# Kernel tuning notes

Measured on AMD Instinct MI355X. Metric: run time of the kernel, lower is better.

The kernel has to match this reference:

```python
import jax, jax.numpy as jnp
import numpy as np

E = 8            # moe_num_experts
HIDDEN = 1024    # hidden_size
FFN = 4096       # ffn_hidden_size
TOKENS = 8192    # total tokens, pre-sorted by expert; balanced -> TOKENS // E per expert


def setup_inputs() -> dict:
    key = jax.random.key(0)
    k1, k2, k3 = jax.random.split(key, 3)
    x = jax.random.normal(k1, (TOKENS, HIDDEN), dtype=jnp.float32)
    # w1, w2 stored flattened as [E*FFN, HIDDEN], matching create_dmoe_expert_weights' view([-1, columns])
    w1 = jax.random.normal(k2, (E * FFN, HIDDEN), dtype=jnp.float32) * (1.0 / np.sqrt(HIDDEN))
    w2 = jax.random.normal(k3, (E * FFN, HIDDEN), dtype=jnp.float32) * (1.0 / np.sqrt(FFN))
    return {"x": x, "w1": w1, "w2": w2, "num_experts": E}


def reference(x, w1, w2, num_experts):
    # Block-diagonal topology of dMoE SparseMLP: tokens sorted by expert, each
    # expert owns a contiguous FFN slice of w1/w2. Equivalent grouped GEMM:
    #   out_e = gelu(x_e @ w1_e^T) @ w2_e   (megablocks gelu = tanh-approx GELU)
    tokens, hidden = x.shape
    ffn = w1.shape[0] // num_experts
    tpe = tokens // num_experts  # tokens per expert (balanced topology)
    xe = x.reshape(num_experts, tpe, hidden)        # [E, T/E, H]
    w1e = w1.reshape(num_experts, ffn, hidden)      # [E, F, H]
    w2e = w2.reshape(num_experts, ffn, hidden)      # [E, F, H]
    h = jax.nn.gelu(jnp.einsum('eth,efh->etf', xe, w1e), approximate=True)  # sdd + gelu
    out = jnp.einsum('etf,efh->eth', h, w2e)        # dsd
    return out.reshape(tokens, hidden)
```

## Files before the change

kernel.cpp:

```cpp
#include <hip/hip_runtime.h>
#include <hip/hip_bf16.h>
#include <stdint.h>

#define NE 8
#define HID 1024
#define FFN 4096
#define TOK 8192
#define TPE (TOK / NE)

typedef __attribute__((ext_vector_type(8))) short    bf16x8;
typedef __attribute__((ext_vector_type(4))) float    f32x4;
typedef __attribute__((ext_vector_type(4))) unsigned short ushort4v;
typedef __attribute__((ext_vector_type(8))) unsigned short ushort8v;


__device__ __forceinline__ unsigned short f2bf(float f) {
    union { float f; unsigned u; } c; c.f = f;
    unsigned r = c.u + 0x7fffu + ((c.u >> 16) & 1u);
    return (unsigned short)(r >> 16);
}

__device__ __forceinline__ float gelu_tanh(float x) {
    const float c0 = 0.7978845608028654f;
    const float c1 = 0.044715f;
    float u = c0 * (x + c1 * x * x * x);
    float t = 1.0f - 2.0f / (1.0f + __expf(2.0f * u));
    return 0.5f * x * (1.0f + t);
}

typedef const __attribute__((address_space(1))) void gbl_void_t;
typedef __attribute__((address_space(3))) void lds_void_t;

__device__ __forceinline__ void gload_lds16(const void* g, void* l) {
    __builtin_amdgcn_global_load_lds((gbl_void_t*)g, (lds_void_t*)l, 16, 0, 0);
}


__global__ void cvt_f32_bf16(const float* __restrict__ in,
                             unsigned short* __restrict__ out) {
    size_t i = ((size_t)blockIdx.x * blockDim.x + threadIdx.x) * 8;
    f32x4 a = *(const f32x4*)(in + i);
    f32x4 b = *(const f32x4*)(in + i + 4);
    ushort8v o;
#pragma unroll
    for (int j = 0; j < 4; j++) { o[j] = f2bf(a[j]); o[4 + j] = f2bf(b[j]); }
    *(ushort8v*)(out + i) = o;
}


__global__ void transpose_cvt(const float* __restrict__ in,
                              unsigned short* __restrict__ out) {
    __shared__ unsigned short tile[64][65];
    const int e  = blockIdx.z;
    const int f0 = blockIdx.x * 64;
    const int h0 = blockIdx.y * 64;
    const float*     src = in  + (size_t)e * FFN * HID;
    unsigned short*  dst = out + (size_t)e * HID * FFN;
    const int t  = threadIdx.x;
    const int tr = t >> 4;
    const int tc = (t & 15) * 4;
#pragma unroll
    for (int i = 0; i < 4; i++) {
        int f = i * 16 + tr;
        f32x4 v = *(const f32x4*)(src + (size_t)(f0 + f) * HID + h0 + tc);
#pragma unroll
        for (int j = 0; j < 4; j++) tile[f][tc + j] = f2bf(v[j]);
    }
    __syncthreads();
#pragma unroll
    for (int i = 0; i < 4; i++) {
        int h = i * 16 + tr;
        ushort4v o;
#pragma unroll
        for (int j = 0; j < 4; j++) o[j] = tile[tc + j][h];
        *(ushort4v*)(dst + (size_t)(h0 + h) * FFN + f0 + tc) = o;
    }
}


template <int BN, int GX, int GY, bool GELU>
__global__ __launch_bounds__(512, 2)
void gemm8p(const unsigned short* __restrict__ A,
            const unsigned short* __restrict__ B,
            void* __restrict__ Cout, int M, int N, int K) {
    constexpr int BM = 256, BK = 64;
    constexpr int NH = BN / 128;
    constexpr int NI = 2 * NH;
    constexpr int LB = BN / 128;
    constexpr int S  = BN / 8;
    constexpr int ABYTES = BM * BK * 2;
    constexpr int BBYTES = BN * BK * 2;
    constexpr int BUF = ABYTES + BBYTES;
    constexpr int VMC = 2 + 2 * LB;
    constexpr int NWG = NE * GX * GY;

    __shared__ __align__(16) char lds[2 * BUF];

    const int lin = blockIdx.x;
    const int wid = (lin & 7) * (NWG >> 3) + (lin >> 3);
    const int e   = wid / (GX * GY);
    const int rem = wid % (GX * GY);
    const int m0  = (rem % GX) * BM;
    const int n0  = (rem / GX) * BN;

    const size_t K2 = (size_t)K * 2;
    const char* Ae = (const char*)(A + (size_t)e * M * K);
    const char* Be = (const char*)(B + (size_t)e * N * K);

    const int tid  = threadIdx.x;
    const int lane = tid & 63;
    const int w    = tid >> 6;
    const int wr   = w >> 2, wc = w & 3;
    const int fr   = lane & 15, fq = lane >> 4;

    const int rA  = tid >> 3;
    const int kb  = (tid & 7) * 16;
    const int kbs = kb ^ ((rA & 7) << 4);
    const char* aptr = Ae + (size_t)(m0 + rA) * K2 + kbs;
    const int   fB   = (rA / S) * 2 * S + (rA % S);
    const char* bptr = Be + (size_t)(n0 + fB) * K2 + kbs;
    char* dA0 = lds + rA * 128 + kb;
    char* dA1 = dA0 + BUF;
    char* dB0 = lds + ABYTES + fB * 128 + kb;
    char* dB1 = dB0 + BUF;

    auto SA = [&](int au, int kt, char* d) {
        const char* s = aptr + (size_t)kt * 128;
#pragma unroll
        for (int i = 0; i < 2; i++)
            gload_lds16(s + (size_t)(au * 64 + i * 128) * K2,
                        d + (au * 64 + i * 128) * 128);
    };
    auto SB = [&](int bu, int kt, char* d) {
        const char* s = bptr + (size_t)kt * 128;
#pragma unroll
        for (int i = 0; i < LB; i++)
            gload_lds16(s + (size_t)(bu * S + i * 128) * K2,
                        d + (bu * S + i * 128) * 128);
    };

    const int kx0 = (fq * 16) ^ ((lane & 7) << 4);
    const char* paA = lds + (wr * 128 + fr) * 128;
    const char* paB = lds + ABYTES + (wc * (BN / 4) + fr) * 128;
    const char* pa0k0 = paA + kx0;        const char* pa0k1 = paA + (kx0 ^ 64);
    const char* pa1k0 = pa0k0 + BUF;      const char* pa1k1 = pa0k1 + BUF;
    const char* pb0k0 = paB + kx0;        const char* pb0k1 = paB + (kx0 ^ 64);
    const char* pb1k0 = pb0k0 + BUF;      const char* pb1k1 = pb0k1 + BUF;

    f32x4 acc[8][NI];
#pragma unroll
    for (int i = 0; i < 8; i++)
#pragma unroll
        for (int j = 0; j < NI; j++) acc[i][j] = f32x4{0.f, 0.f, 0.f, 0.f};

    bf16x8 a[4][2], b0[NH][2], b1[NH][2];

    auto LDA = [&](const char* p0, const char* p1, int mq) {
#pragma unroll
        for (int mi = 0; mi < 4; mi++) {
            a[mi][0] = *(const bf16x8*)(p0 + mq * 8192 + mi * 2048);
            a[mi][1] = *(const bf16x8*)(p1 + mq * 8192 + mi * 2048);
        }
    };
    auto LDB = [&](const char* p0, const char* p1, int nq, bf16x8 (&bb)[NH][2]) {
#pragma unroll
        for (int ni = 0; ni < NH; ni++) {
            bb[ni][0] = *(const bf16x8*)(p0 + (nq * (BN / 8) + ni * 16) * 128);
            bb[ni][1] = *(const bf16x8*)(p1 + (nq * (BN / 8) + ni * 16) * 128);
        }
    };
    auto MMQ = [&](int mq, int nq, bf16x8 (&bb)[NH][2]) {
        __builtin_amdgcn_s_setprio(1);
#pragma unroll
        for (int mi = 0; mi < 4; mi++)
#pragma unroll
            for (int ni = 0; ni < NH; ni++) {
                f32x4& c = acc[mq * 4 + mi][nq * NH + ni];
                c = __builtin_amdgcn_mfma_f32_16x16x32_bf16(a[mi][0], bb[ni][0], c, 0, 0, 0);
                c = __builtin_amdgcn_mfma_f32_16x16x32_bf16(a[mi][1], bb[ni][1], c, 0, 0, 0);
            }
        __builtin_amdgcn_s_setprio(0);
    };

#define MIDBAR()  __builtin_amdgcn_s_barrier();                                      \
                  asm volatile("s_waitcnt lgkmcnt(0)" ::: "memory");                 \
                  __builtin_amdgcn_sched_barrier(0)
#define ENDBAR()  __builtin_amdgcn_s_barrier();                                      \
                  __builtin_amdgcn_sched_barrier(0)
#define LGHINT()  asm volatile("s_waitcnt lgkmcnt(8)" ::: "memory")
#define VMW()     asm volatile("s_waitcnt vmcnt(%0)" :: "n"(VMC) : "memory")

    const int NT   = K / BK;
    const int NTm1 = NT - 1;

    SA(0, 0, dA0); SB(0, 0, dB0); SB(1, 0, dB0); SA(1, 0, dA0);
    SA(0, 1, dA1); SB(0, 1, dB1); SB(1, 1, dB1);
    VMW();
    __builtin_amdgcn_s_barrier();
    __builtin_amdgcn_sched_barrier(0);

    const int NW = NT / 2;
    for (int ww = 0; ww < NW; ++ww) {
        const int T = 2 * ww;
        const int kt1 = T + 1;
        const int kt2 = (T + 2 < NT) ? T + 2 : NTm1;
        const int kt3 = (T + 3 < NT) ? T + 3 : NTm1;

        LDA(pa0k0, pa0k1, 0); LDB(pb0k0, pb0k1, 0, b0); SA(1, kt1, dA1);
        LGHINT(); MIDBAR(); MMQ(0, 0, b0); ENDBAR();
        LDB(pb0k0, pb0k1, 1, b1); SA(0, kt2, dA0);
        MIDBAR(); MMQ(0, 1, b1); ENDBAR();
        LDA(pa0k0, pa0k1, 1); SB(0, kt2, dB0);
        MIDBAR(); MMQ(1, 1, b1); ENDBAR();
        SB(1, kt2, dB0);
        MIDBAR(); MMQ(1, 0, b0); VMW(); ENDBAR();
        LDA(pa1k0, pa1k1, 0); LDB(pb1k0, pb1k1, 0, b0); SA(1, kt2, dA0);
        LGHINT(); MIDBAR(); MMQ(0, 0, b0); ENDBAR();
        LDB(pb1k0, pb1k1, 1, b1); SA(0, kt3, dA1);
        MIDBAR(); MMQ(0, 1, b1); ENDBAR();
        LDA(pa1k0, pa1k1, 1); SB(0, kt3, dB1);
        MIDBAR(); MMQ(1, 1, b1); ENDBAR();
        SB(1, kt3, dB1);
        MIDBAR(); MMQ(1, 0, b0); VMW(); ENDBAR();
    }
    asm volatile("s_waitcnt vmcnt(0)" ::: "memory");

    const int r0 = m0 + wr * 128 + fq * 4;
    const int c0 = n0 + wc * (BN / 4) + fr;
    if constexpr (GELU) {
        unsigned short* C = (unsigned short*)Cout + (size_t)e * M * N;
#pragma unroll
        for (int mi = 0; mi < 8; mi++)
#pragma unroll
            for (int ni = 0; ni < NI; ni++) {
                int row = r0 + mi * 16, col = c0 + ni * 16;
#pragma unroll
                for (int r = 0; r < 4; r++)
                    C[(size_t)(row + r) * N + col] = f2bf(gelu_tanh(acc[mi][ni][r]));
            }
    } else {
        float* C = (float*)Cout + (size_t)e * M * N;
#pragma unroll
        for (int mi = 0; mi < 8; mi++)
#pragma unroll
            for (int ni = 0; ni < NI; ni++) {
                int row = r0 + mi * 16, col = c0 + ni * 16;
#pragma unroll
                for (int r = 0; r < 4; r++)
                    C[(size_t)(row + r) * N + col] = acc[mi][ni][r];
            }
    }
#undef MIDBAR
#undef ENDBAR
#undef LGHINT
#undef VMW
}


__global__ void fused_fallback(const float* __restrict__ x,
                               const float* __restrict__ w1,
                               const float* __restrict__ w2,
                               float* __restrict__ out) {
    __shared__ float xs[HID];
    __shared__ float hs[FFN];
    const int tok = blockIdx.x;
    const int e   = tok / TPE;
    const float* w1e = w1 + (size_t)e * FFN * HID;
    const float* w2e = w2 + (size_t)e * FFN * HID;
    const int t = threadIdx.x;
    for (int i = t; i < HID; i += 256) xs[i] = x[(size_t)tok * HID + i];
    __syncthreads();
    for (int f = t; f < FFN; f += 256) {
        const float* wr_ = w1e + (size_t)f * HID;
        float s = 0.f;
        for (int k = 0; k < HID; k++) s += xs[k] * wr_[k];
        hs[f] = gelu_tanh(s);
    }
    __syncthreads();
    for (int h = t; h < HID; h += 256) {
        float s = 0.f;
        for (int f = 0; f < FFN; f++) s += hs[f] * w2e[(size_t)f * HID + h];
        out[(size_t)tok * HID + h] = s;
    }
}


extern "C" void kernel_launch(void* const* d_in, const int* in_sizes, int n_in,
                              void* d_out, int out_size, void* d_ws, size_t ws_size,
                              hipStream_t stream) {
    const float* x  = (const float*)d_in[0];
    const float* w1 = (const float*)d_in[1];
    const float* w2 = (const float*)d_in[2];
    float* out = (float*)d_out;

    const size_t XB  = (size_t)TOK * HID * 2;
    const size_t W1B = (size_t)NE * FFN * HID * 2;
    const size_t W2B = W1B;
    const size_t HB  = (size_t)TOK * FFN * 2;
    const size_t need = XB + W1B + W2B + HB;

    if (ws_size >= need) {
        char* ws = (char*)d_ws;
        unsigned short* xb  = (unsigned short*)ws;
        unsigned short* w1b = (unsigned short*)(ws + XB);
        unsigned short* w2t = (unsigned short*)(ws + XB + W1B);
        unsigned short* hb  = (unsigned short*)(ws + XB + W1B + W2B);

        cvt_f32_bf16<<<(TOK * HID) / (256 * 8), 256, 0, stream>>>(x, xb);
        cvt_f32_bf16<<<(NE * FFN * HID) / (256 * 8), 256, 0, stream>>>(w1, w1b);
        transpose_cvt<<<dim3(FFN / 64, HID / 64, NE), 256, 0, stream>>>(w2, w2t);

        gemm8p<256, TPE / 256, FFN / 256, true><<<NE * (TPE / 256) * (FFN / 256), 512, 0, stream>>>(
            xb, w1b, hb, TPE, FFN, HID);
        gemm8p<128, TPE / 256, HID / 128, false><<<NE * (TPE / 256) * (HID / 128), 512, 0, stream>>>(
            hb, w2t, out, TPE, HID, FFN);
    } else {
        fused_fallback<<<TOK, 256, 0, stream>>>(x, w1, w2, out);
    }
}
```

Measured before the change: 237.5 us.

## Restructure GEMM main loop into register-pingpong schedule with two barriers per tile

```diff
diff --git a/kernel.cpp b/kernel.cpp
--- a/kernel.cpp
+++ b/kernel.cpp
@@ -80,9 +80,9 @@
 
 template <int BN, int GX, int GY, bool GELU>
 __global__ __launch_bounds__(512, 2)
-void gemm8p(const unsigned short* __restrict__ A,
-            const unsigned short* __restrict__ B,
-            void* __restrict__ Cout, int M, int N, int K) {
+void gemm_rp(const unsigned short* __restrict__ A,
+             const unsigned short* __restrict__ B,
+             void* __restrict__ Cout, int M, int N, int K) {
     constexpr int BM = 256, BK = 64;
     constexpr int NH = BN / 128;
     constexpr int NI = 2 * NH;
@@ -91,7 +91,7 @@
     constexpr int ABYTES = BM * BK * 2;
     constexpr int BBYTES = BN * BK * 2;
     constexpr int BUF = ABYTES + BBYTES;
-    constexpr int VMC = 2 + 2 * LB;
+    constexpr int LPT = 4 + 2 * LB;
     constexpr int NWG = NE * GX * GY;
 
     __shared__ __align__(16) char lds[2 * BUF];
@@ -153,75 +153,68 @@
 #pragma unroll
         for (int j = 0; j < NI; j++) acc[i][j] = f32x4{0.f, 0.f, 0.f, 0.f};
 
-    bf16x8 a[4][2], b0[NH][2], b1[NH][2];
-
-    auto LDA = [&](const char* p0, const char* p1, int mq) {
+    bf16x8 a[2][4][2], b[2][NH][2];
+
+    auto LDQA = [&](int q, const char* k0p, const char* k1p) {
 #pragma unroll
         for (int mi = 0; mi < 4; mi++) {
-            a[mi][0] = *(const bf16x8*)(p0 + mq * 8192 + mi * 2048);
-            a[mi][1] = *(const bf16x8*)(p1 + mq * 8192 + mi * 2048);
+            a[q][mi][0] = *(const bf16x8*)(k0p + q * 8192 + mi * 2048);
+            a[q][mi][1] = *(const bf16x8*)(k1p + q * 8192 + mi * 2048);
         }
     };
-    auto LDB = [&](const char* p0, const char* p1, int nq, bf16x8 (&bb)[NH][2]) {
+    auto LDQB = [&](int q, const char* k0p, const char* k1p) {
 #pragma unroll
         for (int ni = 0; ni < NH; ni++) {
-            bb[ni][0] = *(const bf16x8*)(p0 + (nq * (BN / 8) + ni * 16) * 128);
-            bb[ni][1] = *(const bf16x8*)(p1 + (nq * (BN / 8) + ni * 16) * 128);
+            b[q][ni][0] = *(const bf16x8*)(k0p + (q * (BN / 8) + ni * 16) * 128);
+            b[q][ni][1] = *(const bf16x8*)(k1p + (q * (BN / 8) + ni * 16) * 128);
         }
     };
-    auto MMQ = [&](int mq, int nq, bf16x8 (&bb)[NH][2]) {
+    auto MMQ = [&](int mq, int nq) {
         __builtin_amdgcn_s_setprio(1);
 #pragma unroll
         for (int mi = 0; mi < 4; mi++)
 #pragma unroll
             for (int ni = 0; ni < NH; ni++) {
                 f32x4& c = acc[mq * 4 + mi][nq * NH + ni];
-                c = __builtin_amdgcn_mfma_f32_16x16x32_bf16(a[mi][0], bb[ni][0], c, 0, 0, 0);
-                c = __builtin_amdgcn_mfma_f32_16x16x32_bf16(a[mi][1], bb[ni][1], c, 0, 0, 0);
+                c = __builtin_amdgcn_mfma_f32_16x16x32_bf16(a[mq][mi][0], b[nq][ni][0], c, 0, 0, 0);
+                c = __builtin_amdgcn_mfma_f32_16x16x32_bf16(a[mq][mi][1], b[nq][ni][1], c, 0, 0, 0);
             }
         __builtin_amdgcn_s_setprio(0);
     };
 
-#define MIDBAR()  __builtin_amdgcn_s_barrier();                                      \
-                  asm volatile("s_waitcnt lgkmcnt(0)" ::: "memory");                 \
-                  __builtin_amdgcn_sched_barrier(0)
-#define ENDBAR()  __builtin_amdgcn_s_barrier();                                      \
-                  __builtin_amdgcn_sched_barrier(0)
-#define LGHINT()  asm volatile("s_waitcnt lgkmcnt(8)" ::: "memory")
-#define VMW()     asm volatile("s_waitcnt vmcnt(%0)" :: "n"(VMC) : "memory")
-
     const int NT   = K / BK;
     const int NTm1 = NT - 1;
 
-    SA(0, 0, dA0); SB(0, 0, dB0); SB(1, 0, dB0); SA(1, 0, dA0);
-    SA(0, 1, dA1); SB(0, 1, dB1); SB(1, 1, dB1);
-    VMW();
+    SA(0, 0, dA0); SA(1, 0, dA0); SB(0, 0, dB0); SB(1, 0, dB0);
+    SA(0, 1, dA1); SA(1, 1, dA1); SB(0, 1, dB1); SB(1, 1, dB1);
+    asm volatile("s_waitcnt vmcnt(%0)" :: "n"(LPT) : "memory");
     __builtin_amdgcn_s_barrier();
     __builtin_amdgcn_sched_barrier(0);
 
-    const int NW = NT / 2;
-    for (int ww = 0; ww < NW; ++ww) {
-        const int T = 2 * ww;
-        const int kt1 = T + 1;
-        const int kt2 = (T + 2 < NT) ? T + 2 : NTm1;
-        const int kt3 = (T + 3 < NT) ? T + 3 : NTm1;
-
-        LDA(pa0k0, pa0k1, 0); LDB(pb0k0, pb0k1, 0, b0); SA(1, kt1, dA1);
-        LGHINT(); MIDBAR(); MMQ(0, 0, b0); ENDBAR();
-        LDB(pb0k0, pb0k1, 1, b1); SA(0, kt2, dA0);
-        MIDBAR(); MMQ(0, 1, b1); ENDBAR();
-        LDA(pa0k0, pa0k1, 1); SB(0, kt2, dB0);
-        MIDBAR(); MMQ(1, 1, b1); ENDBAR();
-        SB(1, kt2, dB0);
-        MIDBAR(); MMQ(1, 0, b0); VMW(); ENDBAR();
-        LDA(pa1k0, pa1k1, 0); LDB(pb1k0, pb1k1, 0, b0); SA(1, kt2, dA0);
-        LGHINT(); MIDBAR(); MMQ(0, 0, b0); ENDBAR();
-        LDB(pb1k0, pb1k1, 1, b1); SA(0, kt3, dA1);
-        MIDBAR(); MMQ(0, 1, b1); ENDBAR();
-        LDA(pa1k0, pa1k1, 1); SB(0, kt3, dB1);
-        MIDBAR(); MMQ(1, 1, b1); ENDBAR();
-        SB(1, kt3, dB1);
-        MIDBAR(); MMQ(1, 0, b0); VMW(); ENDBAR();
+    for (int it = 0; it < NT; ++it) {
+        const bool odd = it & 1;
+        const char* Ak0 = odd ? pa1k0 : pa0k0;
+        const char* Ak1 = odd ? pa1k1 : pa0k1;
+        const char* Bk0 = odd ? pb1k0 : pb0k0;
+        const char* Bk1 = odd ? pb1k1 : pb0k1;
+        char* dA = odd ? dA1 : dA0;
+        char* dB = odd ? dB1 : dB0;
+        const int kt2 = (it + 2 < NT) ? it + 2 : NTm1;
+
+        LDQA(0, Ak0, Ak1); LDQB(0, Bk0, Bk1);
+        MMQ(0, 0);
+        LDQA(1, Ak0, Ak1);
+        MMQ(1, 0);
+        LDQB(1, Bk0, Bk1);
+        asm volatile("s_waitcnt lgkmcnt(0)" ::: "memory");
+        __builtin_amdgcn_s_barrier();
+        __builtin_amdgcn_sched_barrier(0);
+        SA(0, kt2, dA); SA(1, kt2, dA); SB(0, kt2, dB); SB(1, kt2, dB);
+        MMQ(1, 1);
+        MMQ(0, 1);
+        asm volatile("s_waitcnt vmcnt(%0)" :: "n"(LPT) : "memory");
+        __builtin_amdgcn_s_barrier();
+        __builtin_amdgcn_sched_barrier(0);
     }
     asm volatile("s_waitcnt vmcnt(0)" ::: "memory");
 
@@ -250,10 +243,6 @@
                     C[(size_t)(row + r) * N + col] = acc[mi][ni][r];
             }
     }
-#undef MIDBAR
-#undef ENDBAR
-#undef LGHINT
-#undef VMW
 }
 
 
@@ -310,9 +299,9 @@
         cvt_f32_bf16<<<(NE * FFN * HID) / (256 * 8), 256, 0, stream>>>(w1, w1b);
         transpose_cvt<<<dim3(FFN / 64, HID / 64, NE), 256, 0, stream>>>(w2, w2t);
 
-        gemm8p<256, TPE / 256, FFN / 256, true><<<NE * (TPE / 256) * (FFN / 256), 512, 0, stream>>>(
+        gemm_rp<256, TPE / 256, FFN / 256, true><<<NE * (TPE / 256) * (FFN / 256), 512, 0, stream>>>(
             xb, w1b, hb, TPE, FFN, HID);
-        gemm8p<128, TPE / 256, HID / 128, false><<<NE * (TPE / 256) * (HID / 128), 512, 0, stream>>>(
+        gemm_rp<128, TPE / 256, HID / 128, false><<<NE * (TPE / 256) * (HID / 128), 512, 0, stream>>>(
             hb, w2t, out, TPE, HID, FFN);
     } else {
         fused_fallback<<<TOK, 256, 0, stream>>>(x, w1, w2, out);
```

Result: slower. 244.4 us (+2.9%).

## Register-prefetch LDS fragments one phase ahead and halve barriers in GEMM loop

Applied to the files above, without the earlier changes.

```diff
diff --git a/kernel.cpp b/kernel.cpp
--- a/kernel.cpp
+++ b/kernel.cpp
@@ -80,9 +80,9 @@
 
 template <int BN, int GX, int GY, bool GELU>
 __global__ __launch_bounds__(512, 2)
-void gemm8p(const unsigned short* __restrict__ A,
-            const unsigned short* __restrict__ B,
-            void* __restrict__ Cout, int M, int N, int K) {
+void gemm_ra(const unsigned short* __restrict__ A,
+             const unsigned short* __restrict__ B,
+             void* __restrict__ Cout, int M, int N, int K) {
     constexpr int BM = 256, BK = 64;
     constexpr int NH = BN / 128;
     constexpr int NI = 2 * NH;
@@ -91,7 +91,7 @@
     constexpr int ABYTES = BM * BK * 2;
     constexpr int BBYTES = BN * BK * 2;
     constexpr int BUF = ABYTES + BBYTES;
-    constexpr int VMC = 2 + 2 * LB;
+    constexpr int VMC = 2 + LB;
     constexpr int NWG = NE * GX * GY;
 
     __shared__ __align__(16) char lds[2 * BUF];
@@ -153,75 +153,86 @@
 #pragma unroll
         for (int j = 0; j < NI; j++) acc[i][j] = f32x4{0.f, 0.f, 0.f, 0.f};
 
-    bf16x8 a[4][2], b0[NH][2], b1[NH][2];
-
-    auto LDA = [&](const char* p0, const char* p1, int mq) {
+    bf16x8 a0[4][2], a1[4][2], b0[NH][2], b1[NH][2];
+
+    auto RA = [&](bf16x8 (&dst)[4][2], const char* k0, const char* k1, int mq) {
 #pragma unroll
         for (int mi = 0; mi < 4; mi++) {
-            a[mi][0] = *(const bf16x8*)(p0 + mq * 8192 + mi * 2048);
-            a[mi][1] = *(const bf16x8*)(p1 + mq * 8192 + mi * 2048);
+            dst[mi][0] = *(const bf16x8*)(k0 + mq * 8192 + mi * 2048);
+            dst[mi][1] = *(const bf16x8*)(k1 + mq * 8192 + mi * 2048);
         }
     };
-    auto LDB = [&](const char* p0, const char* p1, int nq, bf16x8 (&bb)[NH][2]) {
+    auto RB = [&](bf16x8 (&dst)[NH][2], const char* k0, const char* k1, int nq) {
 #pragma unroll
         for (int ni = 0; ni < NH; ni++) {
-            bb[ni][0] = *(const bf16x8*)(p0 + (nq * (BN / 8) + ni * 16) * 128);
-            bb[ni][1] = *(const bf16x8*)(p1 + (nq * (BN / 8) + ni * 16) * 128);
+            dst[ni][0] = *(const bf16x8*)(k0 + (nq * (BN / 8) + ni * 16) * 128);
+            dst[ni][1] = *(const bf16x8*)(k1 + (nq * (BN / 8) + ni * 16) * 128);
         }
     };
-    auto MMQ = [&](int mq, int nq, bf16x8 (&bb)[NH][2]) {
+    auto MMQ = [&](int mq, int nq, bf16x8 (&aa)[4][2], bf16x8 (&bb)[NH][2]) {
         __builtin_amdgcn_s_setprio(1);
 #pragma unroll
         for (int mi = 0; mi < 4; mi++)
 #pragma unroll
             for (int ni = 0; ni < NH; ni++) {
                 f32x4& c = acc[mq * 4 + mi][nq * NH + ni];
-                c = __builtin_amdgcn_mfma_f32_16x16x32_bf16(a[mi][0], bb[ni][0], c, 0, 0, 0);
-                c = __builtin_amdgcn_mfma_f32_16x16x32_bf16(a[mi][1], bb[ni][1], c, 0, 0, 0);
+                c = __builtin_amdgcn_mfma_f32_16x16x32_bf16(aa[mi][0], bb[ni][0], c, 0, 0, 0);
+                c = __builtin_amdgcn_mfma_f32_16x16x32_bf16(aa[mi][1], bb[ni][1], c, 0, 0, 0);
             }
         __builtin_amdgcn_s_setprio(0);
     };
 
-#define MIDBAR()  __builtin_amdgcn_s_barrier();                                      \
-                  asm volatile("s_waitcnt lgkmcnt(0)" ::: "memory");                 \
+#define PHEND()   asm volatile("s_waitcnt lgkmcnt(0)" ::: "memory");                 \
+                  __builtin_amdgcn_sched_barrier(0);                                 \
+                  __builtin_amdgcn_s_barrier();                                      \
                   __builtin_amdgcn_sched_barrier(0)
-#define ENDBAR()  __builtin_amdgcn_s_barrier();                                      \
-                  __builtin_amdgcn_sched_barrier(0)
-#define LGHINT()  asm volatile("s_waitcnt lgkmcnt(8)" ::: "memory")
 #define VMW()     asm volatile("s_waitcnt vmcnt(%0)" :: "n"(VMC) : "memory")
 
     const int NT   = K / BK;
     const int NTm1 = NT - 1;
 
     SA(0, 0, dA0); SB(0, 0, dB0); SB(1, 0, dB0); SA(1, 0, dA0);
-    SA(0, 1, dA1); SB(0, 1, dB1); SB(1, 1, dB1);
+    SA(0, 1, dA1); SB(0, 1, dB1); SB(1, 1, dB1); SA(1, 1, dA1);
     VMW();
     __builtin_amdgcn_s_barrier();
     __builtin_amdgcn_sched_barrier(0);
+    RA(a0, pa0k0, pa0k1, 0);
+    RB(b0, pb0k0, pb0k1, 0);
+    asm volatile("s_waitcnt lgkmcnt(0)" ::: "memory");
+    __builtin_amdgcn_sched_barrier(0);
+
+    auto do_tile = [&](const char* Ak0, const char* Ak1,
+                       const char* Bk0, const char* Bk1,
+                       const char* Ak0n, const char* Ak1n,
+                       const char* Bk0n, const char* Bk1n,
+                       char* dA, char* dB, int kt2) {
+        MMQ(0, 0, a0, b0);
+        RB(b1, Bk0, Bk1, 1);
+        SA(0, kt2, dA); SB(0, kt2, dB);
+        PHEND();
+        MMQ(0, 1, a0, b1);
+        RA(a1, Ak0, Ak1, 1);
+        SB(1, kt2, dB);
+        PHEND();
+        MMQ(1, 1, a1, b1);
+        RA(a0, Ak0n, Ak1n, 0);
+        SA(1, kt2, dA);
+        PHEND();
+        MMQ(1, 0, a1, b0);
+        RB(b0, Bk0n, Bk1n, 0);
+        VMW();
+        PHEND();
+    };
 
     const int NW = NT / 2;
     for (int ww = 0; ww < NW; ++ww) {
         const int T = 2 * ww;
-        const int kt1 = T + 1;
         const int kt2 = (T + 2 < NT) ? T + 2 : NTm1;
         const int kt3 = (T + 3 < NT) ? T + 3 : NTm1;
-
-        LDA(pa0k0, pa0k1, 0); LDB(pb0k0, pb0k1, 0, b0); SA(1, kt1, dA1);
-        LGHINT(); MIDBAR(); MMQ(0, 0, b0); ENDBAR();
-        LDB(pb0k0, pb0k1, 1, b1); SA(0, kt2, dA0);
-        MIDBAR(); MMQ(0, 1, b1); ENDBAR();
-        LDA(pa0k0, pa0k1, 1); SB(0, kt2, dB0);
-        MIDBAR(); MMQ(1, 1, b1); ENDBAR();
-        SB(1, kt2, dB0);
-        MIDBAR(); MMQ(1, 0, b0); VMW(); ENDBAR();
-        LDA(pa1k0, pa1k1, 0); LDB(pb1k0, pb1k1, 0, b0); SA(1, kt2, dA0);
-        LGHINT(); MIDBAR(); MMQ(0, 0, b0); ENDBAR();
-        LDB(pb1k0, pb1k1, 1, b1); SA(0, kt3, dA1);
-        MIDBAR(); MMQ(0, 1, b1); ENDBAR();
-        LDA(pa1k0, pa1k1, 1); SB(0, kt3, dB1);
-        MIDBAR(); MMQ(1, 1, b1); ENDBAR();
-        SB(1, kt3, dB1);
-        MIDBAR(); MMQ(1, 0, b0); VMW(); ENDBAR();
+        do_tile(pa0k0, pa0k1, pb0k0, pb0k1,
+                pa1k0, pa1k1, pb1k0, pb1k1, dA0, dB0, kt2);
+        do_tile(pa1k0, pa1k1, pb1k0, pb1k1,
+                pa0k0, pa0k1, pb0k0, pb0k1, dA1, dB1, kt3);
     }
     asm volatile("s_waitcnt vmcnt(0)" ::: "memory");
 
@@ -250,9 +261,7 @@
                     C[(size_t)(row + r) * N + col] = acc[mi][ni][r];
             }
     }
-#undef MIDBAR
-#undef ENDBAR
-#undef LGHINT
+#undef PHEND
 #undef VMW
 }
 
@@ -310,9 +319,9 @@
         cvt_f32_bf16<<<(NE * FFN * HID) / (256 * 8), 256, 0, stream>>>(w1, w1b);
         transpose_cvt<<<dim3(FFN / 64, HID / 64, NE), 256, 0, stream>>>(w2, w2t);
 
-        gemm8p<256, TPE / 256, FFN / 256, true><<<NE * (TPE / 256) * (FFN / 256), 512, 0, stream>>>(
+        gemm_ra<256, TPE / 256, FFN / 256, true><<<NE * (TPE / 256) * (FFN / 256), 512, 0, stream>>>(
             xb, w1b, hb, TPE, FFN, HID);
-        gemm8p<128, TPE / 256, HID / 128, false><<<NE * (TPE / 256) * (HID / 128), 512, 0, stream>>>(
+        gemm_ra<128, TPE / 256, HID / 128, false><<<NE * (TPE / 256) * (HID / 128), 512, 0, stream>>>(
             hb, w2t, out, TPE, HID, FFN);
     } else {
         fused_fallback<<<TOK, 256, 0, stream>>>(x, w1, w2, out);
```

New measurement: 243.1 us. +2.4%, slower.

## Fuse fp32-to-bf16 conversion of x and w1 into first GEMM's register-staged loads

Applied to the files above, without the earlier changes.

```diff
diff --git a/kernel.cpp b/kernel.cpp
--- a/kernel.cpp
+++ b/kernel.cpp
@@ -33,18 +33,6 @@
 
 __device__ __forceinline__ void gload_lds16(const void* g, void* l) {
     __builtin_amdgcn_global_load_lds((gbl_void_t*)g, (lds_void_t*)l, 16, 0, 0);
-}
-
-
-__global__ void cvt_f32_bf16(const float* __restrict__ in,
-                             unsigned short* __restrict__ out) {
-    size_t i = ((size_t)blockIdx.x * blockDim.x + threadIdx.x) * 8;
-    f32x4 a = *(const f32x4*)(in + i);
-    f32x4 b = *(const f32x4*)(in + i + 4);
-    ushort8v o;
-#pragma unroll
-    for (int j = 0; j < 4; j++) { o[j] = f2bf(a[j]); o[4 + j] = f2bf(b[j]); }
-    *(ushort8v*)(out + i) = o;
 }
 
 
@@ -75,6 +63,202 @@
         for (int j = 0; j < 4; j++) o[j] = tile[tc + j][h];
         *(ushort4v*)(dst + (size_t)(h0 + h) * FFN + f0 + tc) = o;
     }
+}
+
+
+template <int GX, int GY>
+__global__ __launch_bounds__(512, 2)
+void gemm8f(const float* __restrict__ Af,
+            const float* __restrict__ Bf,
+            unsigned short* __restrict__ Cout, int M, int N, int K) {
+    constexpr int BM = 256, BN = 256, BK = 64;
+    constexpr int NH = 2, NI = 4, S = 32;
+    constexpr int ABYTES = BM * BK * 2;
+    constexpr int BBYTES = BN * BK * 2;
+    constexpr int BUF = ABYTES + BBYTES;
+    constexpr int NWG = NE * GX * GY;
+
+    __shared__ __align__(16) char lds[2 * BUF];
+
+    const int lin = blockIdx.x;
+    const int wid = (lin & 7) * (NWG >> 3) + (lin >> 3);
+    const int e   = wid / (GX * GY);
+    const int rem = wid % (GX * GY);
+    const int m0  = (rem % GX) * BM;
+    const int n0  = (rem / GX) * BN;
+
+    const float* Ae = Af + (size_t)e * M * K;
+    const float* Be = Bf + (size_t)e * N * K;
+
+    const int tid  = threadIdx.x;
+    const int lane = tid & 63;
+    const int w    = tid >> 6;
+    const int wr   = w >> 2, wc = w & 3;
+    const int fr   = lane & 15, fq = lane >> 4;
+
+    const int rA  = tid >> 3;
+    const int kb  = (tid & 7) * 16;
+    const int kbs = kb ^ ((rA & 7) << 4);
+    const int eoff = kbs >> 1;
+    const float* aFb = Ae + (size_t)(m0 + rA) * K + eoff;
+    const int   fB   = (rA / S) * 2 * S + (rA % S);
+    const float* bFb = Be + (size_t)(n0 + fB) * K + eoff;
+    char* dA0 = lds + rA * 128 + kb;
+    char* dA1 = dA0 + BUF;
+    char* dB0 = lds + ABYTES + fB * 128 + kb;
+    char* dB1 = dB0 + BUF;
+
+    auto LD_A = [&](int au, int kt, f32x4 (&g)[4]) {
+        const float* s = aFb + (size_t)kt * 64;
+        g[0] = *(const f32x4*)(s + (size_t)(au * 64) * K);
+        g[1] = *(const f32x4*)(s + (size_t)(au * 64) * K + 4);
+        g[2] = *(const f32x4*)(s + (size_t)(au * 64 + 128) * K);
+        g[3] = *(const f32x4*)(s + (size_t)(au * 64 + 128) * K + 4);
+    };
+    auto LD_B = [&](int bu, int kt, f32x4 (&g)[4]) {
+        const float* s = bFb + (size_t)kt * 64;
+        g[0] = *(const f32x4*)(s + (size_t)(bu * S) * K);
+        g[1] = *(const f32x4*)(s + (size_t)(bu * S) * K + 4);
+        g[2] = *(const f32x4*)(s + (size_t)(bu * S + 128) * K);
+        g[3] = *(const f32x4*)(s + (size_t)(bu * S + 128) * K + 4);
+    };
+    auto PACK = [&](const f32x4& lo, const f32x4& hi) {
+        ushort8v o;
+#pragma unroll
+        for (int j = 0; j < 4; j++) { o[j] = f2bf(lo[j]); o[4 + j] = f2bf(hi[j]); }
+        return o;
+    };
+    auto WR_A = [&](int au, char* d, f32x4 (&g)[4]) {
+        *(ushort8v*)(d + (au * 64) * 128)       = PACK(g[0], g[1]);
+        *(ushort8v*)(d + (au * 64 + 128) * 128) = PACK(g[2], g[3]);
+    };
+    auto WR_B = [&](int bu, char* d, f32x4 (&g)[4]) {
+        *(ushort8v*)(d + (bu * S) * 128)        = PACK(g[0], g[1]);
+        *(ushort8v*)(d + (bu * S + 128) * 128)  = PACK(g[2], g[3]);
+    };
+
+    const int kx0 = (fq * 16) ^ ((lane & 7) << 4);
+    const char* paA = lds + (wr * 128 + fr) * 128;
+    const char* paB = lds + ABYTES + (wc * (BN / 4) + fr) * 128;
+    const char* pa0k0 = paA + kx0;        const char* pa0k1 = paA + (kx0 ^ 64);
+    const char* pa1k0 = pa0k0 + BUF;      const char* pa1k1 = pa0k1 + BUF;
+    const char* pb0k0 = paB + kx0;        const char* pb0k1 = paB + (kx0 ^ 64);
+    const char* pb1k0 = pb0k0 + BUF;      const char* pb1k1 = pb0k1 + BUF;
+
+    bf16x8 a[4][2], b0[NH][2], b1[NH][2];
+
+    auto LDA = [&](const char* p0, const char* p1, int mq) {
+#pragma unroll
+        for (int mi = 0; mi < 4; mi++) {
+            a[mi][0] = *(const bf16x8*)(p0 + mq * 8192 + mi * 2048);
+            a[mi][1] = *(const bf16x8*)(p1 + mq * 8192 + mi * 2048);
+        }
+    };
+    auto LDB = [&](const char* p0, const char* p1, int nq, bf16x8 (&bb)[NH][2]) {
+#pragma unroll
+        for (int ni = 0; ni < NH; ni++) {
+            bb[ni][0] = *(const bf16x8*)(p0 + (nq * (BN / 8) + ni * 16) * 128);
+            bb[ni][1] = *(const bf16x8*)(p1 + (nq * (BN / 8) + ni * 16) * 128);
+        }
+    };
+
+    f32x4 acc[8][NI];
+
+    auto MMQ = [&](int mq, int nq, bf16x8 (&bb)[NH][2]) {
+        __builtin_amdgcn_s_setprio(1);
+#pragma unroll
+        for (int mi = 0; mi < 4; mi++)
+#pragma unroll
+            for (int ni = 0; ni < NH; ni++) {
+                f32x4& c = acc[mq * 4 + mi][nq * NH + ni];
+                c = __builtin_amdgcn_mfma_f32_16x16x32_bf16(a[mi][0], bb[ni][0], c, 0, 0, 0);
+                c = __builtin_amdgcn_mfma_f32_16x16x32_bf16(a[mi][1], bb[ni][1], c, 0, 0, 0);
+            }
+        __builtin_amdgcn_s_setprio(0);
+    };
+
+#define MIDBAR()  __builtin_amdgcn_s_barrier();                                      \
+                  asm volatile("s_waitcnt lgkmcnt(0)" ::: "memory")
+#define ENDBAR()  __builtin_amdgcn_s_barrier()
+#define LGHINT()  asm volatile("s_waitcnt lgkmcnt(8)" ::: "memory")
+
+    const int NT   = K / BK;
+    const int NTm1 = NT - 1;
+
+    f32x4 gO[4], gE[4];
+    {
+        f32x4 t0[4];
+        LD_A(0, 0, t0); WR_A(0, dA0, t0);
+        LD_A(1, 0, t0); WR_A(1, dA0, t0);
+        LD_B(0, 0, t0); WR_B(0, dB0, t0);
+        LD_B(1, 0, t0); WR_B(1, dB0, t0);
+        LD_A(0, 1, t0); WR_A(0, dA1, t0);
+        LD_B(0, 1, t0); WR_B(0, dB1, t0);
+        LD_B(1, 1, t0); WR_B(1, dB1, t0);
+    }
+    LD_A(1, 1, gO);
+    LD_A(0, (2 < NT ? 2 : NTm1), gE);
+#pragma unroll
+    for (int i = 0; i < 8; i++)
+#pragma unroll
+        for (int j = 0; j < NI; j++) acc[i][j] = f32x4{0.f, 0.f, 0.f, 0.f};
+    asm volatile("s_waitcnt lgkmcnt(0)" ::: "memory");
+    __builtin_amdgcn_s_barrier();
+
+    const int NW = NT / 2;
+    for (int ww = 0; ww < NW; ++ww) {
+        const int T = 2 * ww;
+        const int kt2 = (T + 2 < NT) ? T + 2 : NTm1;
+        const int kt3 = (T + 3 < NT) ? T + 3 : NTm1;
+        const int kt4 = (T + 4 < NT) ? T + 4 : NTm1;
+
+        LDA(pa0k0, pa0k1, 0); LDB(pb0k0, pb0k1, 0, b0); LGHINT();
+        MIDBAR();
+        WR_A(1, dA1, gO); LD_B(0, kt2, gO);
+        MMQ(0, 0, b0); ENDBAR();
+        LDB(pb0k0, pb0k1, 1, b1);
+        MIDBAR();
+        WR_A(0, dA0, gE); LD_B(1, kt2, gE);
+        MMQ(0, 1, b1); ENDBAR();
+        LDA(pa0k0, pa0k1, 1);
+        MIDBAR();
+        WR_B(0, dB0, gO); LD_A(1, kt2, gO);
+        MMQ(1, 1, b1); ENDBAR();
+        MIDBAR();
+        WR_B(1, dB0, gE); LD_A(0, kt3, gE);
+        MMQ(1, 0, b0); ENDBAR();
+        LDA(pa1k0, pa1k1, 0); LDB(pb1k0, pb1k1, 0, b0); LGHINT();
+        MIDBAR();
+        WR_A(1, dA0, gO); LD_B(0, kt3, gO);
+        MMQ(0, 0, b0); ENDBAR();
+        LDB(pb1k0, pb1k1, 1, b1);
+        MIDBAR();
+        WR_A(0, dA1, gE); LD_B(1, kt3, gE);
+        MMQ(0, 1, b1); ENDBAR();
+        LDA(pa1k0, pa1k1, 1);
+        MIDBAR();
+        WR_B(0, dB1, gO); LD_A(1, kt3, gO);
+        MMQ(1, 1, b1); ENDBAR();
+        MIDBAR();
+        WR_B(1, dB1, gE); LD_A(0, kt4, gE);
+        MMQ(1, 0, b0); ENDBAR();
+    }
+
+    const int r0 = m0 + wr * 128 + fq * 4;
+    const int c0 = n0 + wc * (BN / 4) + fr;
+    unsigned short* C = Cout + (size_t)e * M * N;
+#pragma unroll
+    for (int mi = 0; mi < 8; mi++)
+#pragma unroll
+        for (int ni = 0; ni < NI; ni++) {
+            int row = r0 + mi * 16, col = c0 + ni * 16;
+#pragma unroll
+            for (int r = 0; r < 4; r++)
+                C[(size_t)(row + r) * N + col] = f2bf(gelu_tanh(acc[mi][ni][r]));
+        }
+#undef MIDBAR
+#undef ENDBAR
+#undef LGHINT
 }
 
 
@@ -183,10 +367,8 @@
     };
 
 #define MIDBAR()  __builtin_amdgcn_s_barrier();                                      \
-                  asm volatile("s_waitcnt lgkmcnt(0)" ::: "memory");                 \
-                  __builtin_amdgcn_sched_barrier(0)
-#define ENDBAR()  __builtin_amdgcn_s_barrier();                                      \
-                  __builtin_amdgcn_sched_barrier(0)
+                  asm volatile("s_waitcnt lgkmcnt(0)" ::: "memory")
+#define ENDBAR()  __builtin_amdgcn_s_barrier()
 #define LGHINT()  asm volatile("s_waitcnt lgkmcnt(8)" ::: "memory")
 #define VMW()     asm volatile("s_waitcnt vmcnt(%0)" :: "n"(VMC) : "memory")
 
@@ -197,7 +379,6 @@
     SA(0, 1, dA1); SB(0, 1, dB1); SB(1, 1, dB1);
     VMW();
     __builtin_amdgcn_s_barrier();
-    __builtin_amdgcn_sched_barrier(0);
 
     const int NW = NT / 2;
     for (int ww = 0; ww < NW; ++ww) {
@@ -206,16 +387,16 @@
         const int kt2 = (T + 2 < NT) ? T + 2 : NTm1;
         const int kt3 = (T + 3 < NT) ? T + 3 : NTm1;
 
-        LDA(pa0k0, pa0k1, 0); LDB(pb0k0, pb0k1, 0, b0); SA(1, kt1, dA1);
-        LGHINT(); MIDBAR(); MMQ(0, 0, b0); ENDBAR();
+        LDA(pa0k0, pa0k1, 0); LDB(pb0k0, pb0k1, 0, b0); SA(1, kt1, dA1); LGHINT();
+        MIDBAR(); MMQ(0, 0, b0); ENDBAR();
         LDB(pb0k0, pb0k1, 1, b1); SA(0, kt2, dA0);
         MIDBAR(); MMQ(0, 1, b1); ENDBAR();
         LDA(pa0k0, pa0k1, 1); SB(0, kt2, dB0);
         MIDBAR(); MMQ(1, 1, b1); ENDBAR();
         SB(1, kt2, dB0);
         MIDBAR(); MMQ(1, 0, b0); VMW(); ENDBAR();
-        LDA(pa1k0, pa1k1, 0); LDB(pb1k0, pb1k1, 0, b0); SA(1, kt2, dA0);
-        LGHINT(); MIDBAR(); MMQ(0, 0, b0); ENDBAR();
+        LDA(pa1k0, pa1k1, 0); LDB(pb1k0, pb1k1, 0, b0); SA(1, kt2, dA0); LGHINT();
+        MIDBAR(); MMQ(0, 0, b0); ENDBAR();
         LDB(pb1k0, pb1k1, 1, b1); SA(0, kt3, dA1);
         MIDBAR(); MMQ(0, 1, b1); ENDBAR();
         LDA(pa1k0, pa1k1, 1); SB(0, kt3, dB1);
@@ -293,25 +474,19 @@
     const float* w2 = (const float*)d_in[2];
     float* out = (float*)d_out;
 
-    const size_t XB  = (size_t)TOK * HID * 2;
-    const size_t W1B = (size_t)NE * FFN * HID * 2;
-    const size_t W2B = W1B;
+    const size_t W2B = (size_t)NE * FFN * HID * 2;
     const size_t HB  = (size_t)TOK * FFN * 2;
-    const size_t need = XB + W1B + W2B + HB;
+    const size_t need = W2B + HB;
 
     if (ws_size >= need) {
         char* ws = (char*)d_ws;
-        unsigned short* xb  = (unsigned short*)ws;
-        unsigned short* w1b = (unsigned short*)(ws + XB);
-        unsigned short* w2t = (unsigned short*)(ws + XB + W1B);
-        unsigned short* hb  = (unsigned short*)(ws + XB + W1B + W2B);
-
-        cvt_f32_bf16<<<(TOK * HID) / (256 * 8), 256, 0, stream>>>(x, xb);
-        cvt_f32_bf16<<<(NE * FFN * HID) / (256 * 8), 256, 0, stream>>>(w1, w1b);
+        unsigned short* w2t = (unsigned short*)ws;
+        unsigned short* hb  = (unsigned short*)(ws + W2B);
+
         transpose_cvt<<<dim3(FFN / 64, HID / 64, NE), 256, 0, stream>>>(w2, w2t);
 
-        gemm8p<256, TPE / 256, FFN / 256, true><<<NE * (TPE / 256) * (FFN / 256), 512, 0, stream>>>(
-            xb, w1b, hb, TPE, FFN, HID);
+        gemm8f<TPE / 256, FFN / 256><<<NE * (TPE / 256) * (FFN / 256), 512, 0, stream>>>(
+            x, w1, hb, TPE, FFN, HID);
         gemm8p<128, TPE / 256, HID / 128, false><<<NE * (TPE / 256) * (HID / 128), 512, 0, stream>>>(
             hb, w2t, out, TPE, HID, FFN);
     } else {
```

Result: no change. 233.0 us (median of 2 runs) (-1.9%).
